# Kernel optimization log

Hardware: AMD Instinct MI355X
Metric: run time of the kernel (lower is better)

## Reference

```python
import jax, jax.numpy as jnp
import numpy as np

N_NODES = 100000
N_EDGES = 1600000
HID = 64
EDGE_DIM = 32
N_LAYERS = 3
BN_EPS = 1e-5


def setup_inputs() -> dict:
    key = jax.random.key(0)
    ks = jax.random.split(key, 8)
    x = jax.random.normal(ks[0], (N_NODES, HID), dtype=jnp.float32)
    edge_index = jax.random.randint(ks[1], (2, N_EDGES), 0, N_NODES, dtype=jnp.int32)
    edge_attr = jax.random.normal(ks[2], (N_EDGES, EDGE_DIM), dtype=jnp.float32)
    s = 0.1  # small init scale for numerical stability
    We = jax.random.normal(ks[3], (N_LAYERS, EDGE_DIM, HID), dtype=jnp.float32) * s
    be = jnp.zeros((N_LAYERS, HID), jnp.float32)
    W1 = jax.random.normal(ks[4], (N_LAYERS, HID, HID), dtype=jnp.float32) * s
    b1 = jnp.zeros((N_LAYERS, HID), jnp.float32)
    W2 = jax.random.normal(ks[5], (N_LAYERS, HID, HID), dtype=jnp.float32) * s
    b2 = jnp.zeros((N_LAYERS, HID), jnp.float32)
    gamma = jnp.ones((N_LAYERS, HID), jnp.float32)
    beta = jnp.zeros((N_LAYERS, HID), jnp.float32)
    Wout = jax.random.normal(ks[6], (HID, HID), dtype=jnp.float32) * s
    bout = jnp.zeros((HID,), jnp.float32)
    return {"x": x, "edge_index": edge_index, "edge_attr": edge_attr,
            "We": We, "be": be, "W1": W1, "b1": b1, "W2": W2, "b2": b2,
            "gamma": gamma, "beta": beta, "Wout": Wout, "bout": bout}


def _forward(x, edge_index, edge_attr, We, be, W1, b1, W2, b2, gamma, beta, Wout, bout):
    src = edge_index[0]  # x_j (source of message)
    dst = edge_index[1]  # aggregation target
    n = x.shape[0]
    for i in range(N_LAYERS):
        # GINEConv: message = relu(x_j + lin_edge(edge_attr)); scatter-add to dst
        e = edge_attr @ We[i] + be[i]                      # [E, H]
        m = jax.nn.relu(x[src] + e)                        # [E, H] (dominant traffic)
        agg = jax.ops.segment_sum(m, dst, num_segments=n)  # [N, H]
        h = x + agg                                        # (1 + eps)*x, eps = 0
        # 2-layer MLP
        h = jax.nn.relu(h @ W1[i] + b1[i]) @ W2[i] + b2[i]
        # BatchNorm1d (training mode: batch statistics, biased variance)
        mean = jnp.mean(h, axis=0)
        var = jnp.var(h, axis=0)
        h = (h - mean) * jax.lax.rsqrt(var + BN_EPS) * gamma[i] + beta[i]
        x = jax.nn.relu(h)
    return x @ Wout + bout


def reference(x, edge_index, edge_attr, We, be, W1, b1, W2, b2, gamma, beta, Wout, bout):
    return _forward(x, edge_index, edge_attr, We, be, W1, b1, W2, b2, gamma, beta, Wout, bout)
```

## Files before the change

kernel.cpp:

```cpp
#include <hip/hip_runtime.h>

#define N_NODES 100000
#define N_EDGES 1600000
#define HID 64
#define EDIM 32
#define BN_EPS 1e-5f

#define SCAN_CHUNK 1024
#define NB_SCAN ((N_NODES + SCAN_CHUNK - 1) / SCAN_CHUNK)

#define G_NODES 16
#define CAP 320

__global__ __launch_bounds__(256) void hist_kernel(
    const int* __restrict__ dst, int* __restrict__ cnt)
{
    int i = (int)(blockIdx.x * blockDim.x + threadIdx.x);
    const int stride = (int)(gridDim.x * blockDim.x);
    for (; i < N_EDGES; i += stride) atomicAdd(&cnt[dst[i]], 1);
}

__global__ __launch_bounds__(256) void scan1_kernel(
    const int* __restrict__ cnt, int* __restrict__ bsum)
{
    __shared__ int s[256];
    const int b = (int)blockIdx.x, t = (int)threadIdx.x;
    const int base = b * SCAN_CHUNK + t * 4;
    int sum = 0;
#pragma unroll
    for (int k = 0; k < 4; ++k) {
        int idx = base + k;
        if (idx < N_NODES) sum += cnt[idx];
    }
    s[t] = sum;
    __syncthreads();
    for (int off = 128; off > 0; off >>= 1) {
        if (t < off) s[t] += s[t + off];
        __syncthreads();
    }
    if (t == 0) bsum[b] = s[0];
}

__global__ __launch_bounds__(128) void scan2_kernel(
    const int* __restrict__ bsum, int* __restrict__ bofs, int* __restrict__ row_ptr)
{
    __shared__ int s[128];
    const int t = (int)threadIdx.x;
    const int v = (t < NB_SCAN) ? bsum[t] : 0;
    s[t] = v;
    __syncthreads();
    for (int off = 1; off < 128; off <<= 1) {
        int add = (t >= off) ? s[t - off] : 0;
        __syncthreads();
        s[t] += add;
        __syncthreads();
    }
    if (t < NB_SCAN) bofs[t] = s[t] - v;
    if (t == NB_SCAN - 1) row_ptr[N_NODES] = s[t];
}

__global__ __launch_bounds__(256) void scan3_kernel(
    const int* __restrict__ cnt, const int* __restrict__ bofs,
    int* __restrict__ row_ptr, int* __restrict__ pos)
{
    __shared__ int s[256];
    const int b = (int)blockIdx.x, t = (int)threadIdx.x;
    const int base = b * SCAN_CHUNK + t * 4;
    int v[4];
    int sum = 0;
#pragma unroll
    for (int k = 0; k < 4; ++k) {
        int idx = base + k;
        v[k] = (idx < N_NODES) ? cnt[idx] : 0;
        sum += v[k];
    }
    s[t] = sum;
    __syncthreads();
    for (int off = 1; off < 256; off <<= 1) {
        int add = (t >= off) ? s[t - off] : 0;
        __syncthreads();
        s[t] += add;
        __syncthreads();
    }
    int run = s[t] - sum + bofs[b];
#pragma unroll
    for (int k = 0; k < 4; ++k) {
        int idx = base + k;
        if (idx < N_NODES) {
            row_ptr[idx] = run;
            pos[idx] = run;
            run += v[k];
        }
    }
}

__global__ __launch_bounds__(256) void scatter_kernel(
    const int* __restrict__ src, const int* __restrict__ dst,
    int* __restrict__ pos, int* __restrict__ perm_e, int* __restrict__ perm_src)
{
    int i = (int)(blockIdx.x * blockDim.x + threadIdx.x);
    const int stride = (int)(gridDim.x * blockDim.x);
    for (; i < N_EDGES; i += stride) {
        const int d = dst[i];
        const int p = atomicAdd(&pos[d], 1);
        perm_e[p] = i;
        perm_src[p] = src[i];
    }
}

__global__ __launch_bounds__(256) void gather_staged_kernel(
    const float* __restrict__ x, const float* __restrict__ eattr,
    const int* __restrict__ row_ptr, const int* __restrict__ perm_e,
    const int* __restrict__ perm_src,
    const float* __restrict__ We, const float* __restrict__ be,
    float* __restrict__ agg)
{
    __shared__ float s_attr[CAP * EDIM];
    __shared__ int   s_src[CAP];

    const int tid  = (int)threadIdx.x;
    const int lane = tid & 63;
    const int w    = tid >> 6;
    const int node_lo = (int)blockIdx.x * G_NODES;

    float wv[EDIM];
#pragma unroll
    for (int k = 0; k < EDIM; ++k) wv[k] = We[k * HID + lane];
    const float bias = be[lane];

    int rp[5];
#pragma unroll
    for (int i = 0; i < 5; ++i) {
        int n = node_lo + 4 * w + i;
        rp[i] = row_ptr[n < N_NODES ? n : N_NODES];
    }
    float acc[4] = {0.0f, 0.0f, 0.0f, 0.0f};

    const int e0 = row_ptr[node_lo < N_NODES ? node_lo : N_NODES];
    const int hi = node_lo + G_NODES;
    const int e1 = row_ptr[hi < N_NODES ? hi : N_NODES];

    for (int c0 = e0; c0 < e1; c0 += CAP) {
        const int cnt = (e1 - c0 < CAP) ? (e1 - c0) : CAP;
        __syncthreads();
        for (int i = tid; i < cnt * 8; i += 256) {
            const int row = i >> 3, part = i & 7;
            const int ep = perm_e[c0 + row];
            ((float4*)s_attr)[i] = ((const float4*)eattr)[(size_t)ep * 8 + part];
        }
        for (int i = tid; i < cnt; i += 256) s_src[i] = perm_src[c0 + i];
        __syncthreads();
        const int c1 = c0 + cnt;

#pragma unroll
        for (int q = 0; q < 4; ++q) {
            const int jb = (rp[q]     > c0) ? rp[q]     : c0;
            const int je = (rp[q + 1] < c1) ? rp[q + 1] : c1;
            float a = acc[q];
            int j = jb;
            if (j < je) {
                int s0 = s_src[j - c0];
                float xv = x[(size_t)s0 * HID + lane];
                while (j < je) {
                    const float4* p = (const float4*)(s_attr + (size_t)(j - c0) * EDIM);
                    const int jn = j + 1;
                    float xn = 0.0f;
                    if (jn < je) {
                        const int sn = s_src[jn - c0];
                        xn = x[(size_t)sn * HID + lane];
                    }
                    float e = bias;
#pragma unroll
                    for (int jj = 0; jj < 8; ++jj) {
                        const float4 qv = p[jj];
                        e = fmaf(qv.x, wv[4 * jj + 0], e);
                        e = fmaf(qv.y, wv[4 * jj + 1], e);
                        e = fmaf(qv.z, wv[4 * jj + 2], e);
                        e = fmaf(qv.w, wv[4 * jj + 3], e);
                    }
                    a += fmaxf(xv + e, 0.0f);
                    xv = xn;
                    j = jn;
                }
            }
            acc[q] = a;
        }
    }

#pragma unroll
    for (int q = 0; q < 4; ++q) {
        const int n = node_lo + 4 * w + q;
        if (n < N_NODES) agg[(size_t)n * HID + lane] = acc[q];
    }
}

__global__ __launch_bounds__(256) void mlp_kernel(
    const float* __restrict__ xin, const float* __restrict__ agg,
    const float* __restrict__ W1, const float* __restrict__ b1,
    const float* __restrict__ W2, const float* __restrict__ b2,
    float* __restrict__ uout)
{
    const int lane = threadIdx.x & 63;
    const int wid  = (int)((blockIdx.x * blockDim.x + threadIdx.x) >> 6);
    const int n    = wid * 64 + lane;
    const bool ok  = (n < N_NODES);
    const size_t base = (size_t)n * HID;

    float h[HID];
    if (ok) {
        const float4* px = (const float4*)(xin + base);
        const float4* pa = (const float4*)(agg + base);
#pragma unroll
        for (int j = 0; j < HID / 4; ++j) {
            float4 xv = px[j];
            float4 av = pa[j];
            h[4 * j + 0] = xv.x + av.x;
            h[4 * j + 1] = xv.y + av.y;
            h[4 * j + 2] = xv.z + av.z;
            h[4 * j + 3] = xv.w + av.w;
        }
    } else {
#pragma unroll
        for (int k = 0; k < HID; ++k) h[k] = 0.0f;
    }

    float u[HID];
#pragma unroll
    for (int f = 0; f < HID; ++f) u[f] = b2[f];

    for (int c = 0; c < 4; ++c) {
        float t[16];
#pragma unroll
        for (int j = 0; j < 16; ++j) t[j] = b1[c * 16 + j];
#pragma unroll
        for (int k = 0; k < HID; ++k) {
            const float hk = h[k];
#pragma unroll
            for (int j = 0; j < 16; ++j)
                t[j] = fmaf(hk, W1[k * HID + c * 16 + j], t[j]);
        }
#pragma unroll
        for (int j = 0; j < 16; ++j) t[j] = fmaxf(t[j], 0.0f);
#pragma unroll
        for (int j = 0; j < 16; ++j) {
            const float tj = t[j];
#pragma unroll
            for (int f = 0; f < HID; ++f)
                u[f] = fmaf(tj, W2[(c * 16 + j) * HID + f], u[f]);
        }
    }

    if (ok) {
        float4* po = (float4*)(uout + base);
#pragma unroll
        for (int j = 0; j < HID / 4; ++j)
            po[j] = make_float4(u[4 * j], u[4 * j + 1], u[4 * j + 2], u[4 * j + 3]);
    }
}

__global__ __launch_bounds__(256) void out_kernel(
    const float* __restrict__ xin, const float* __restrict__ Wo,
    const float* __restrict__ bo, float* __restrict__ out)
{
    const int lane = threadIdx.x & 63;
    const int wid  = (int)((blockIdx.x * blockDim.x + threadIdx.x) >> 6);
    const int n    = wid * 64 + lane;
    const bool ok  = (n < N_NODES);
    const size_t base = (size_t)n * HID;

    float h[HID];
    if (ok) {
        const float4* px = (const float4*)(xin + base);
#pragma unroll
        for (int j = 0; j < HID / 4; ++j) {
            float4 xv = px[j];
            h[4 * j + 0] = xv.x; h[4 * j + 1] = xv.y;
            h[4 * j + 2] = xv.z; h[4 * j + 3] = xv.w;
        }
    } else {
#pragma unroll
        for (int k = 0; k < HID; ++k) h[k] = 0.0f;
    }

    for (int c = 0; c < 4; ++c) {
        float t[16];
#pragma unroll
        for (int j = 0; j < 16; ++j) t[j] = bo[c * 16 + j];
#pragma unroll
        for (int k = 0; k < HID; ++k) {
            const float hk = h[k];
#pragma unroll
            for (int j = 0; j < 16; ++j)
                t[j] = fmaf(hk, Wo[k * HID + c * 16 + j], t[j]);
        }
        if (ok) {
            float4* po = (float4*)(out + base + c * 16);
#pragma unroll
            for (int j = 0; j < 4; ++j)
                po[j] = make_float4(t[4 * j], t[4 * j + 1], t[4 * j + 2], t[4 * j + 3]);
        }
    }
}

__global__ __launch_bounds__(256) void stats_kernel(
    const float* __restrict__ u, float* __restrict__ stats)
{
    __shared__ float ls[256];
    __shared__ float ls2[256];
    const int tid = (int)threadIdx.x;
    const int g   = (int)(blockIdx.x * 256 + tid);
    const int f   = g & 63;
    const int row = g >> 6;
    const int rstride = (int)((gridDim.x * 256) >> 6);

    float s = 0.0f, s2 = 0.0f;
    for (int n = row; n < N_NODES; n += rstride) {
        float v = u[(size_t)n * HID + f];
        s += v;
        s2 = fmaf(v, v, s2);
    }
    ls[tid] = s;
    ls2[tid] = s2;
    __syncthreads();
    if (tid < 64) {
        float a = ls[tid] + ls[tid + 64] + ls[tid + 128] + ls[tid + 192];
        float b = ls2[tid] + ls2[tid + 64] + ls2[tid + 128] + ls2[tid + 192];
        atomicAdd(&stats[tid], a);
        atomicAdd(&stats[64 + tid], b);
    }
}

__global__ __launch_bounds__(256) void bn_relu_kernel(
    const float* __restrict__ u, const float* __restrict__ stats,
    const float* __restrict__ gamma, const float* __restrict__ beta,
    float* __restrict__ xout)
{
    const int total4 = N_NODES * HID / 4;
    int i = (int)(blockIdx.x * blockDim.x + threadIdx.x);
    const int stride = (int)(gridDim.x * blockDim.x);
    const int fb = (i * 4) & 63;

    const float invN = 1.0f / (float)N_NODES;
    float sc[4], sh[4];
#pragma unroll
    for (int j = 0; j < 4; ++j) {
        float mean = stats[fb + j] * invN;
        float var  = stats[64 + fb + j] * invN - mean * mean;
        float s    = gamma[fb + j] * rsqrtf(var + BN_EPS);
        sc[j] = s;
        sh[j] = beta[fb + j] - mean * s;
    }
    for (; i < total4; i += stride) {
        float4 v = ((const float4*)u)[i];
        v.x = fmaxf(fmaf(v.x, sc[0], sh[0]), 0.0f);
        v.y = fmaxf(fmaf(v.y, sc[1], sh[1]), 0.0f);
        v.z = fmaxf(fmaf(v.z, sc[2], sh[2]), 0.0f);
        v.w = fmaxf(fmaf(v.w, sc[3], sh[3]), 0.0f);
        ((float4*)xout)[i] = v;
    }
}

extern "C" void kernel_launch(void* const* d_in, const int* in_sizes, int n_in,
                              void* d_out, int out_size, void* d_ws, size_t ws_size,
                              hipStream_t stream)
{
    const float* x0    = (const float*)d_in[0];
    const int*   eidx  = (const int*)d_in[1];
    const float* eattr = (const float*)d_in[2];
    const float* We    = (const float*)d_in[3];
    const float* be    = (const float*)d_in[4];
    const float* W1    = (const float*)d_in[5];
    const float* b1    = (const float*)d_in[6];
    const float* W2    = (const float*)d_in[7];
    const float* b2    = (const float*)d_in[8];
    const float* gamma = (const float*)d_in[9];
    const float* beta  = (const float*)d_in[10];
    const float* Wout  = (const float*)d_in[11];
    const float* bout  = (const float*)d_in[12];
    float* out = (float*)d_out;

    const int* src = eidx;
    const int* dst = eidx + N_EDGES;

    const size_t NH = (size_t)N_NODES * HID;

    float* A     = (float*)d_ws;
    float* AGG   = A + NH;
    float* stats = AGG + NH;
    int* cnt      = (int*)(stats + 128);
    int* bsum     = cnt + N_NODES;
    int* bofs     = bsum + 128;
    int* row_ptr  = bofs + 128;
    int* pos      = row_ptr + N_NODES + 1;
    int* perm_e   = pos + N_NODES;
    int* perm_src = perm_e + N_EDGES;
    float* B = out;

    hipMemsetAsync(cnt, 0, N_NODES * sizeof(int), stream);
    hist_kernel<<<1024, 256, 0, stream>>>(dst, cnt);
    scan1_kernel<<<NB_SCAN, 256, 0, stream>>>(cnt, bsum);
    scan2_kernel<<<1, 128, 0, stream>>>(bsum, bofs, row_ptr);
    scan3_kernel<<<NB_SCAN, 256, 0, stream>>>(cnt, bofs, row_ptr, pos);
    scatter_kernel<<<1024, 256, 0, stream>>>(src, dst, pos, perm_e, perm_src);

    const int mlp_blocks    = ((N_NODES + 63) / 64 + 3) / 4;
    const int gather_blocks = (N_NODES + G_NODES - 1) / G_NODES;

    const float* xin = x0;
    for (int i = 0; i < 3; ++i) {
        hipMemsetAsync(stats, 0, 128 * sizeof(float), stream);

        gather_staged_kernel<<<gather_blocks, 256, 0, stream>>>(
            xin, eattr, row_ptr, perm_e, perm_src,
            We + (size_t)i * EDIM * HID, be + (size_t)i * HID, AGG);

        mlp_kernel<<<mlp_blocks, 256, 0, stream>>>(
            xin, AGG,
            W1 + (size_t)i * HID * HID, b1 + (size_t)i * HID,
            W2 + (size_t)i * HID * HID, b2 + (size_t)i * HID, B);

        stats_kernel<<<256, 256, 0, stream>>>(B, stats);

        bn_relu_kernel<<<1024, 256, 0, stream>>>(
            B, stats, gamma + (size_t)i * HID, beta + (size_t)i * HID, A);

        xin = A;
    }

    out_kernel<<<mlp_blocks, 256, 0, stream>>>(A, Wout, bout, out);
}
```

Measured before the change: 1.749 ms.

## Stage edge attributes via direct global-to-LDS loads with deeper x prefetch

Edge attributes and source indices are now copied into LDS with global_load_lds, so the data skips registers. The perm_e indices for the next chunk are loaded ahead of time. The chunk size is halved and the kernel gets an occupancy hint of 5 blocks per CU, aiming for more concurrent blocks. x rows are prefetched three edges ahead across the node boundaries inside a chunk, and the 32-term dot product is split into four partial sums to shorten the dependency chain. The trade-offs are more register pressure from the eps array and more chunk iterations with barriers.

```diff
diff --git a/kernel.cpp b/kernel.cpp
--- a/kernel.cpp
+++ b/kernel.cpp
@@ -10,7 +10,10 @@
 #define NB_SCAN ((N_NODES + SCAN_CHUNK - 1) / SCAN_CHUNK)
 
 #define G_NODES 16
-#define CAP 320
+#define CAP 160
+#define S_ATTR_F4 (CAP * 8 + 64)
+#define S_SRC_I   (CAP + 64)
+#define N_EPS ((CAP * 8 + 255) / 256)
 
 __global__ __launch_bounds__(256) void hist_kernel(
     const int* __restrict__ dst, int* __restrict__ cnt)
@@ -108,15 +111,28 @@
     }
 }
 
-__global__ __launch_bounds__(256) void gather_staged_kernel(
+__device__ __forceinline__ void gl_lds16(const float4* g, float4* l)
+{
+    __builtin_amdgcn_global_load_lds(
+        (const __attribute__((address_space(1))) void*)g,
+        (__attribute__((address_space(3))) void*)l, 16, 0, 0);
+}
+__device__ __forceinline__ void gl_lds4(const int* g, int* l)
+{
+    __builtin_amdgcn_global_load_lds(
+        (const __attribute__((address_space(1))) void*)g,
+        (__attribute__((address_space(3))) void*)l, 4, 0, 0);
+}
+
+__global__ __launch_bounds__(256, 5) void gather_staged_kernel(
     const float* __restrict__ x, const float* __restrict__ eattr,
     const int* __restrict__ row_ptr, const int* __restrict__ perm_e,
     const int* __restrict__ perm_src,
     const float* __restrict__ We, const float* __restrict__ be,
     float* __restrict__ agg)
 {
-    __shared__ float s_attr[CAP * EDIM];
-    __shared__ int   s_src[CAP];
+    __shared__ float4 s_attr[S_ATTR_F4];
+    __shared__ int    s_src[S_SRC_I];
 
     const int tid  = (int)threadIdx.x;
     const int lane = tid & 63;
@@ -136,54 +152,93 @@
     }
     float acc[4] = {0.0f, 0.0f, 0.0f, 0.0f};
 
-    const int e0 = row_ptr[node_lo < N_NODES ? node_lo : N_NODES];
+    const int e0 = row_ptr[node_lo];
     const int hi = node_lo + G_NODES;
     const int e1 = row_ptr[hi < N_NODES ? hi : N_NODES];
 
+    const float4* eattr4 = (const float4*)eattr;
+
+    int eps[N_EPS];
+    auto load_eps = [&](int cbase) {
+        const int cc  = (e1 - cbase < CAP) ? (e1 - cbase) : CAP;
+        const int nqq = cc * 8;
+#pragma unroll
+        for (int k = 0; k < N_EPS; ++k) {
+            int i = w * 64 + k * 256 + lane;
+            if (i >= nqq) i = nqq - 1;
+            eps[k] = perm_e[cbase + (i >> 3)];
+        }
+    };
+
+    if (e0 < e1) load_eps(e0);
+
     for (int c0 = e0; c0 < e1; c0 += CAP) {
         const int cnt = (e1 - c0 < CAP) ? (e1 - c0) : CAP;
-        __syncthreads();
-        for (int i = tid; i < cnt * 8; i += 256) {
-            const int row = i >> 3, part = i & 7;
-            const int ep = perm_e[c0 + row];
-            ((float4*)s_attr)[i] = ((const float4*)eattr)[(size_t)ep * 8 + part];
-        }
-        for (int i = tid; i < cnt; i += 256) s_src[i] = perm_src[c0 + i];
-        __syncthreads();
-        const int c1 = c0 + cnt;
-
-#pragma unroll
-        for (int q = 0; q < 4; ++q) {
-            const int jb = (rp[q]     > c0) ? rp[q]     : c0;
-            const int je = (rp[q + 1] < c1) ? rp[q + 1] : c1;
-            float a = acc[q];
-            int j = jb;
-            if (j < je) {
-                int s0 = s_src[j - c0];
-                float xv = x[(size_t)s0 * HID + lane];
-                while (j < je) {
-                    const float4* p = (const float4*)(s_attr + (size_t)(j - c0) * EDIM);
-                    const int jn = j + 1;
-                    float xn = 0.0f;
-                    if (jn < je) {
-                        const int sn = s_src[jn - c0];
-                        xn = x[(size_t)sn * HID + lane];
-                    }
-                    float e = bias;
+        const int nq  = cnt * 8;
+        const int c1  = c0 + cnt;
+
+        __syncthreads();
+
+#pragma unroll
+        for (int k = 0; k < N_EPS; ++k) {
+            const int b = w * 64 + k * 256;
+            if (b < nq) {
+                int i = b + lane;
+                if (i >= nq) i = nq - 1;
+                gl_lds16(eattr4 + (size_t)eps[k] * 8 + (i & 7), s_attr + b);
+            }
+        }
+        {
+            const int b = w * 64;
+            if (b < cnt) {
+                int i = b + lane;
+                if (i >= cnt) i = cnt - 1;
+                gl_lds4(perm_src + c0 + i, s_src + b);
+            }
+        }
+        if (c0 + CAP < e1) load_eps(c0 + CAP);
+
+        __syncthreads();
+
+        int f0 = rp[0] > c0 ? rp[0] : c0;
+        const int F1 = rp[4] < c1 ? rp[4] : c1;
+        if (f0 < F1) {
+            const int FL = F1 - 1;
+            int j1 = (f0 + 1 > FL) ? FL : f0 + 1;
+            int j2 = (f0 + 2 > FL) ? FL : f0 + 2;
+            const int sA = s_src[f0 - c0];
+            const int sB = s_src[j1 - c0];
+            int si = s_src[j2 - c0];
+            float xq0 = x[(size_t)sA * HID + lane];
+            float xq1 = x[(size_t)sB * HID + lane];
+
+#pragma unroll
+            for (int q = 0; q < 4; ++q) {
+                const int jb = (rp[q]     > c0) ? rp[q]     : c0;
+                const int je = (rp[q + 1] < c1) ? rp[q + 1] : c1;
+                float a = acc[q];
+                for (int j = jb; j < je; ++j) {
+                    const float xl = x[(size_t)si * HID + lane];
+                    int j3 = j + 3; if (j3 > FL) j3 = FL;
+                    si = s_src[j3 - c0];
+
+                    const float4* p = s_attr + (size_t)(j - c0) * 8;
+                    float ee[4] = {bias, 0.0f, 0.0f, 0.0f};
 #pragma unroll
                     for (int jj = 0; jj < 8; ++jj) {
                         const float4 qv = p[jj];
-                        e = fmaf(qv.x, wv[4 * jj + 0], e);
-                        e = fmaf(qv.y, wv[4 * jj + 1], e);
-                        e = fmaf(qv.z, wv[4 * jj + 2], e);
-                        e = fmaf(qv.w, wv[4 * jj + 3], e);
+                        float t = ee[jj & 3];
+                        t = fmaf(qv.x, wv[4 * jj + 0], t);
+                        t = fmaf(qv.y, wv[4 * jj + 1], t);
+                        t = fmaf(qv.z, wv[4 * jj + 2], t);
+                        t = fmaf(qv.w, wv[4 * jj + 3], t);
+                        ee[jj & 3] = t;
                     }
-                    a += fmaxf(xv + e, 0.0f);
-                    xv = xn;
-                    j = jn;
+                    a += fmaxf(xq0 + ((ee[0] + ee[1]) + (ee[2] + ee[3])), 0.0f);
+                    xq0 = xq1; xq1 = xl;
                 }
+                acc[q] = a;
             }
-            acc[q] = a;
         }
     }
 
```

After: 1.604 ms. -8.3%, faster.

## Replace LDS-staged edge gather with per-wave scalar-load software pipeline

Applied to the files above, without the earlier changes.

Rewrites the GINE gather kernel. The shared-memory staging of edge attributes and the block-wide barriers are removed. Each wave now walks its four nodes' CSR edge range serially, loading each edge's 32-float attribute row with s_load_dwordx16 into scalar registers. Those loads are double-buffered, and the perm_e, perm_src and x loads run ahead of the current edge. Per-node sums come from differencing one running prefix sum at row boundaries, which avoids per-node loop overhead but can lose some float precision. Scalar-cache throughput and the serial latency chain are the main risks.

```diff
diff --git a/kernel.cpp b/kernel.cpp
--- a/kernel.cpp
+++ b/kernel.cpp
@@ -10,7 +10,8 @@
 #define NB_SCAN ((N_NODES + SCAN_CHUNK - 1) / SCAN_CHUNK)
 
 #define G_NODES 16
-#define CAP 320
+
+typedef __attribute__((ext_vector_type(16))) float f32x16;
 
 __global__ __launch_bounds__(256) void hist_kernel(
     const int* __restrict__ dst, int* __restrict__ cnt)
@@ -108,89 +109,143 @@
     }
 }
 
-__global__ __launch_bounds__(256) void gather_staged_kernel(
+#define SWAIT() do { asm volatile("s_waitcnt lgkmcnt(0)" ::: "memory"); \
+                     __builtin_amdgcn_sched_barrier(0); } while (0)
+
+__device__ __forceinline__ float edge_step(
+    int j, int FL,
+    const float* __restrict__ eattr, const int* __restrict__ perm_e,
+    const int* __restrict__ perm_src, const float* __restrict__ x,
+    int lane, const float* __restrict__ wv, float bias,
+    f32x16& cl, f32x16& ch,
+    f32x16& nl, f32x16& nh,
+    int& eN, int& sN,
+    float& xq0, float& xq1)
+{
+    SWAIT();
+    const float* ap = eattr + (size_t)(unsigned)eN * EDIM;
+    int j2 = j + 2; if (j2 > FL) j2 = FL;
+    int j3 = j + 3; if (j3 > FL) j3 = FL;
+    int e_out, s_out;
+    asm volatile(
+        "s_load_dwordx16 %0, %4, 0x0\n\t"
+        "s_load_dwordx16 %1, %4, 0x40\n\t"
+        "s_load_dword    %2, %5, 0x0\n\t"
+        "s_load_dword    %3, %6, 0x0"
+        : "=&s"(nl), "=&s"(nh), "=&s"(e_out), "=&s"(s_out)
+        : "s"(ap), "s"(perm_e + j2), "s"(perm_src + j3));
+
+    const float xq2 = x[(size_t)(unsigned)sN * HID + lane];
+
+    float ee0 = bias, ee1 = 0.0f, ee2 = 0.0f, ee3 = 0.0f;
+#pragma unroll
+    for (int k = 0; k < 16; k += 4) {
+        ee0 = fmaf(cl[k + 0], wv[k + 0], ee0);
+        ee1 = fmaf(cl[k + 1], wv[k + 1], ee1);
+        ee2 = fmaf(cl[k + 2], wv[k + 2], ee2);
+        ee3 = fmaf(cl[k + 3], wv[k + 3], ee3);
+    }
+#pragma unroll
+    for (int k = 0; k < 16; k += 4) {
+        ee0 = fmaf(ch[k + 0], wv[16 + k + 0], ee0);
+        ee1 = fmaf(ch[k + 1], wv[16 + k + 1], ee1);
+        ee2 = fmaf(ch[k + 2], wv[16 + k + 2], ee2);
+        ee3 = fmaf(ch[k + 3], wv[16 + k + 3], ee3);
+    }
+    const float c = fmaxf(xq0 + ((ee0 + ee1) + (ee2 + ee3)), 0.0f);
+    xq0 = xq1; xq1 = xq2;
+    eN = e_out; sN = s_out;
+    return c;
+}
+
+__global__ __launch_bounds__(256, 6) void gather_csr_kernel(
     const float* __restrict__ x, const float* __restrict__ eattr,
     const int* __restrict__ row_ptr, const int* __restrict__ perm_e,
     const int* __restrict__ perm_src,
     const float* __restrict__ We, const float* __restrict__ be,
     float* __restrict__ agg)
 {
-    __shared__ float s_attr[CAP * EDIM];
-    __shared__ int   s_src[CAP];
-
     const int tid  = (int)threadIdx.x;
     const int lane = tid & 63;
-    const int w    = tid >> 6;
-    const int node_lo = (int)blockIdx.x * G_NODES;
+    const int w    = __builtin_amdgcn_readfirstlane(tid >> 6);
+    const int node_lo = (int)blockIdx.x * G_NODES + 4 * w;
 
     float wv[EDIM];
 #pragma unroll
     for (int k = 0; k < EDIM; ++k) wv[k] = We[k * HID + lane];
     const float bias = be[lane];
 
-    int rp[5];
+    int rpv[5];
 #pragma unroll
     for (int i = 0; i < 5; ++i) {
-        int n = node_lo + 4 * w + i;
-        rp[i] = row_ptr[n < N_NODES ? n : N_NODES];
-    }
-    float acc[4] = {0.0f, 0.0f, 0.0f, 0.0f};
-
-    const int e0 = row_ptr[node_lo < N_NODES ? node_lo : N_NODES];
-    const int hi = node_lo + G_NODES;
-    const int e1 = row_ptr[hi < N_NODES ? hi : N_NODES];
-
-    for (int c0 = e0; c0 < e1; c0 += CAP) {
-        const int cnt = (e1 - c0 < CAP) ? (e1 - c0) : CAP;
-        __syncthreads();
-        for (int i = tid; i < cnt * 8; i += 256) {
-            const int row = i >> 3, part = i & 7;
-            const int ep = perm_e[c0 + row];
-            ((float4*)s_attr)[i] = ((const float4*)eattr)[(size_t)ep * 8 + part];
-        }
-        for (int i = tid; i < cnt; i += 256) s_src[i] = perm_src[c0 + i];
-        __syncthreads();
-        const int c1 = c0 + cnt;
-
-#pragma unroll
-        for (int q = 0; q < 4; ++q) {
-            const int jb = (rp[q]     > c0) ? rp[q]     : c0;
-            const int je = (rp[q + 1] < c1) ? rp[q + 1] : c1;
-            float a = acc[q];
-            int j = jb;
-            if (j < je) {
-                int s0 = s_src[j - c0];
-                float xv = x[(size_t)s0 * HID + lane];
-                while (j < je) {
-                    const float4* p = (const float4*)(s_attr + (size_t)(j - c0) * EDIM);
-                    const int jn = j + 1;
-                    float xn = 0.0f;
-                    if (jn < je) {
-                        const int sn = s_src[jn - c0];
-                        xn = x[(size_t)sn * HID + lane];
-                    }
-                    float e = bias;
-#pragma unroll
-                    for (int jj = 0; jj < 8; ++jj) {
-                        const float4 qv = p[jj];
-                        e = fmaf(qv.x, wv[4 * jj + 0], e);
-                        e = fmaf(qv.y, wv[4 * jj + 1], e);
-                        e = fmaf(qv.z, wv[4 * jj + 2], e);
-                        e = fmaf(qv.w, wv[4 * jj + 3], e);
-                    }
-                    a += fmaxf(xv + e, 0.0f);
-                    xv = xn;
-                    j = jn;
-                }
-            }
-            acc[q] = a;
-        }
-    }
-
+        int n = node_lo + i;
+        n = (n < N_NODES) ? n : N_NODES;
+        rpv[i] = __builtin_amdgcn_readfirstlane(row_ptr[n]);
+    }
+    const int F0 = rpv[0], rp1 = rpv[1], rp2 = rpv[2], rp3 = rpv[3], F1 = rpv[4];
+
+    float a = 0.0f, sn1 = 0.0f, sn2 = 0.0f, sn3 = 0.0f;
+
+    if (F0 < F1) {
+        const int FL = F1 - 1;
+        f32x16 A0, A1, B0, B1;
+        int eN, sN;
+        float xq0, xq1;
+
+        {
+            int jB = F0 + 1; if (jB > FL) jB = FL;
+            int jC = F0 + 2; if (jC > FL) jC = FL;
+            int e0i, eNi, s0i, s1i, sNi;
+            asm volatile(
+                "s_load_dword %0, %5, 0x0\n\t"
+                "s_load_dword %1, %6, 0x0\n\t"
+                "s_load_dword %2, %7, 0x0\n\t"
+                "s_load_dword %3, %8, 0x0\n\t"
+                "s_load_dword %4, %9, 0x0"
+                : "=&s"(e0i), "=&s"(eNi), "=&s"(s0i), "=&s"(s1i), "=&s"(sNi)
+                : "s"(perm_e + F0), "s"(perm_e + jB), "s"(perm_src + F0),
+                  "s"(perm_src + jB), "s"(perm_src + jC));
+            SWAIT();
+            const float* ap0 = eattr + (size_t)(unsigned)e0i * EDIM;
+            asm volatile(
+                "s_load_dwordx16 %0, %2, 0x0\n\t"
+                "s_load_dwordx16 %1, %2, 0x40"
+                : "=&s"(A0), "=&s"(A1) : "s"(ap0));
+            xq0 = x[(size_t)(unsigned)s0i * HID + lane];
+            xq1 = x[(size_t)(unsigned)s1i * HID + lane];
+            eN = eNi; sN = sNi;
+        }
+
+        int j = F0;
+        while (true) {
+            a += edge_step(j, FL, eattr, perm_e, perm_src, x, lane, wv, bias,
+                           A0, A1, B0, B1, eN, sN, xq0, xq1);
+            ++j;
+            if (j == rp1) sn1 = a;
+            if (j == rp2) sn2 = a;
+            if (j == rp3) sn3 = a;
+            if (j >= F1) break;
+
+            a += edge_step(j, FL, eattr, perm_e, perm_src, x, lane, wv, bias,
+                           B0, B1, A0, A1, eN, sN, xq0, xq1);
+            ++j;
+            if (j == rp1) sn1 = a;
+            if (j == rp2) sn2 = a;
+            if (j == rp3) sn3 = a;
+            if (j >= F1) break;
+        }
+        SWAIT();
+    }
+
+    float r[4];
+    r[0] = sn1;
+    r[1] = sn2 - sn1;
+    r[2] = sn3 - sn2;
+    r[3] = a - sn3;
 #pragma unroll
     for (int q = 0; q < 4; ++q) {
-        const int n = node_lo + 4 * w + q;
-        if (n < N_NODES) agg[(size_t)n * HID + lane] = acc[q];
+        const int n = node_lo + q;
+        if (n < N_NODES) agg[(size_t)n * HID + lane] = r[q];
     }
 }
 
@@ -410,7 +465,7 @@
     for (int i = 0; i < 3; ++i) {
         hipMemsetAsync(stats, 0, 128 * sizeof(float), stream);
 
-        gather_staged_kernel<<<gather_blocks, 256, 0, stream>>>(
+        gather_csr_kernel<<<gather_blocks, 256, 0, stream>>>(
             xin, eattr, row_ptr, perm_e, perm_src,
             We + (size_t)i * EDIM * HID, be + (size_t)i * HID, AGG);
 
```

Result: faster. 1.618 ms (-7.5%).

## Pre-permute edge attributes into CSR order and stream gather without LDS staging

Applied to the files above, without the earlier changes.

Adds a one-time kernel that copies edge_attr into dst-sorted order in workspace, so all three layer gathers read attributes linearly instead of through perm_e indirection. The gather kernel drops shared-memory staging and syncthreads. Each wave instead walks its 4 nodes' contiguous edge range with a software-pipelined prefetch of x rows and source indices, and derives per-node sums from running prefix snapshots. It also splits the edge-linear FMA chain into four accumulators and sets a higher occupancy hint. The cost is an extra 200MB permute pass plus workspace use, with a fallback path when the workspace is too small.

```diff
diff --git a/kernel.cpp b/kernel.cpp
--- a/kernel.cpp
+++ b/kernel.cpp
@@ -1,4 +1,5 @@
 #include <hip/hip_runtime.h>
+#include <stdint.h>
 
 #define N_NODES 100000
 #define N_EDGES 1600000
@@ -10,7 +11,6 @@
 #define NB_SCAN ((N_NODES + SCAN_CHUNK - 1) / SCAN_CHUNK)
 
 #define G_NODES 16
-#define CAP 320
 
 __global__ __launch_bounds__(256) void hist_kernel(
     const int* __restrict__ dst, int* __restrict__ cnt)
@@ -108,89 +108,119 @@
     }
 }
 
-__global__ __launch_bounds__(256) void gather_staged_kernel(
-    const float* __restrict__ x, const float* __restrict__ eattr,
+__global__ __launch_bounds__(256) void permute_attr_kernel(
+    const float* __restrict__ eattr, const int* __restrict__ perm_e,
+    float* __restrict__ outp)
+{
+    const int total = N_EDGES * 8;
+    int i = (int)(blockIdx.x * blockDim.x + threadIdx.x);
+    const int stride = (int)(gridDim.x * blockDim.x);
+    for (; i < total; i += stride) {
+        const int row = i >> 3, part = i & 7;
+        ((float4*)outp)[i] =
+            ((const float4*)eattr)[(size_t)(unsigned)perm_e[row] * 8 + part];
+    }
+}
+
+template<bool LINEAR>
+__global__ __launch_bounds__(256, 4) void gather_kernel(
+    const float* __restrict__ x, const float* __restrict__ attr,
     const int* __restrict__ row_ptr, const int* __restrict__ perm_e,
     const int* __restrict__ perm_src,
     const float* __restrict__ We, const float* __restrict__ be,
     float* __restrict__ agg)
 {
-    __shared__ float s_attr[CAP * EDIM];
-    __shared__ int   s_src[CAP];
-
     const int tid  = (int)threadIdx.x;
     const int lane = tid & 63;
-    const int w    = tid >> 6;
-    const int node_lo = (int)blockIdx.x * G_NODES;
-
-    float wv[EDIM];
-#pragma unroll
-    for (int k = 0; k < EDIM; ++k) wv[k] = We[k * HID + lane];
-    const float bias = be[lane];
-
-    int rp[5];
+    const int w    = __builtin_amdgcn_readfirstlane(tid >> 6);
+    const int node_lo = (int)blockIdx.x * G_NODES + 4 * w;
+
+    int rpv[5];
 #pragma unroll
     for (int i = 0; i < 5; ++i) {
-        int n = node_lo + 4 * w + i;
-        rp[i] = row_ptr[n < N_NODES ? n : N_NODES];
-    }
-    float acc[4] = {0.0f, 0.0f, 0.0f, 0.0f};
-
-    const int e0 = row_ptr[node_lo < N_NODES ? node_lo : N_NODES];
-    const int hi = node_lo + G_NODES;
-    const int e1 = row_ptr[hi < N_NODES ? hi : N_NODES];
-
-    for (int c0 = e0; c0 < e1; c0 += CAP) {
-        const int cnt = (e1 - c0 < CAP) ? (e1 - c0) : CAP;
-        __syncthreads();
-        for (int i = tid; i < cnt * 8; i += 256) {
-            const int row = i >> 3, part = i & 7;
-            const int ep = perm_e[c0 + row];
-            ((float4*)s_attr)[i] = ((const float4*)eattr)[(size_t)ep * 8 + part];
-        }
-        for (int i = tid; i < cnt; i += 256) s_src[i] = perm_src[c0 + i];
-        __syncthreads();
-        const int c1 = c0 + cnt;
-
-#pragma unroll
-        for (int q = 0; q < 4; ++q) {
-            const int jb = (rp[q]     > c0) ? rp[q]     : c0;
-            const int je = (rp[q + 1] < c1) ? rp[q + 1] : c1;
-            float a = acc[q];
-            int j = jb;
-            if (j < je) {
-                int s0 = s_src[j - c0];
-                float xv = x[(size_t)s0 * HID + lane];
-                while (j < je) {
-                    const float4* p = (const float4*)(s_attr + (size_t)(j - c0) * EDIM);
-                    const int jn = j + 1;
-                    float xn = 0.0f;
-                    if (jn < je) {
-                        const int sn = s_src[jn - c0];
-                        xn = x[(size_t)sn * HID + lane];
-                    }
-                    float e = bias;
-#pragma unroll
-                    for (int jj = 0; jj < 8; ++jj) {
-                        const float4 qv = p[jj];
-                        e = fmaf(qv.x, wv[4 * jj + 0], e);
-                        e = fmaf(qv.y, wv[4 * jj + 1], e);
-                        e = fmaf(qv.z, wv[4 * jj + 2], e);
-                        e = fmaf(qv.w, wv[4 * jj + 3], e);
-                    }
-                    a += fmaxf(xv + e, 0.0f);
-                    xv = xn;
-                    j = jn;
+        int n = node_lo + i;
+        n = (n < N_NODES) ? n : N_NODES;
+        rpv[i] = __builtin_amdgcn_readfirstlane(row_ptr[n]);
+    }
+    const int F0 = rpv[0], rp1 = rpv[1], rp2 = rpv[2], rp3 = rpv[3], F1 = rpv[4];
+
+    float a = 0.0f, sn1 = 0.0f, sn2 = 0.0f, sn3 = 0.0f;
+
+    if (F0 < F1) {
+        const int FL = F1 - 1;
+
+        float pf_prev;
+        {
+            int gl = F0 + lane; if (gl > FL) gl = FL;
+            size_t row = LINEAR ? (size_t)gl : (size_t)(unsigned)perm_e[gl];
+            pf_prev = attr[row * EDIM];
+        }
+
+        float wv[EDIM];
+#pragma unroll
+        for (int k = 0; k < EDIM; ++k) wv[k] = We[k * HID + lane];
+        const float bias = be[lane];
+
+        int jA = F0;
+        int jB = F0 + 1; if (jB > FL) jB = FL;
+        int jC = F0 + 2; if (jC > FL) jC = FL;
+        const int s0 = perm_src[jA];
+        const int s1 = perm_src[jB];
+        int sN = perm_src[jC];
+        float xq0 = x[(size_t)(unsigned)s0 * HID + lane];
+        float xq1 = x[(size_t)(unsigned)s1 * HID + lane];
+
+        for (int gb = F0; gb < F1; gb += 64) {
+            const int gend = (gb + 64 < F1) ? gb + 64 : F1;
+
+            float pf = 0.0f;
+            if (gb + 64 < F1) {
+                int gl = gb + 64 + lane; if (gl > FL) gl = FL;
+                size_t row = LINEAR ? (size_t)gl : (size_t)(unsigned)perm_e[gl];
+                pf = attr[row * EDIM];
+            }
+
+#pragma unroll 2
+            for (int j = gb; j < gend; ++j) {
+                const float xq2 = x[(size_t)(unsigned)sN * HID + lane];
+                int j3 = j + 3; if (j3 > FL) j3 = FL;
+                sN = perm_src[j3];
+
+                size_t row = LINEAR ? (size_t)j : (size_t)(unsigned)perm_e[j];
+                const float4* ap = (const float4*)(attr + row * EDIM);
+
+                float e0 = bias, e1 = 0.0f, e2 = 0.0f, e3 = 0.0f;
+#pragma unroll
+                for (int k = 0; k < 8; ++k) {
+                    const float4 q = ap[k];
+                    e0 = fmaf(q.x, wv[4 * k + 0], e0);
+                    e1 = fmaf(q.y, wv[4 * k + 1], e1);
+                    e2 = fmaf(q.z, wv[4 * k + 2], e2);
+                    e3 = fmaf(q.w, wv[4 * k + 3], e3);
                 }
+                a += fmaxf(xq0 + ((e0 + e1) + (e2 + e3)), 0.0f);
+                xq0 = xq1; xq1 = xq2;
+
+                if (j + 1 == rp1) sn1 = a;
+                if (j + 1 == rp2) sn2 = a;
+                if (j + 1 == rp3) sn3 = a;
             }
-            acc[q] = a;
-        }
-    }
-
+
+            asm volatile("" :: "v"(pf_prev));
+            pf_prev = pf;
+        }
+        asm volatile("" :: "v"(pf_prev));
+    }
+
+    float r[4];
+    r[0] = sn1;
+    r[1] = sn2 - sn1;
+    r[2] = sn3 - sn2;
+    r[3] = a - sn3;
 #pragma unroll
     for (int q = 0; q < 4; ++q) {
-        const int n = node_lo + 4 * w + q;
-        if (n < N_NODES) agg[(size_t)n * HID + lane] = acc[q];
+        const int n = node_lo + q;
+        if (n < N_NODES) agg[(size_t)n * HID + lane] = r[q];
     }
 }
 
@@ -396,12 +426,20 @@
     int* perm_src = perm_e + N_EDGES;
     float* B = out;
 
+    uintptr_t eap_off = (((uintptr_t)(perm_src + N_EDGES) - (uintptr_t)d_ws)
+                         + 255) & ~(uintptr_t)255;
+    const size_t need = (size_t)eap_off + (size_t)N_EDGES * EDIM * sizeof(float);
+    const bool lin = (ws_size >= need);
+    float* EAP = (float*)((char*)d_ws + eap_off);
+
     hipMemsetAsync(cnt, 0, N_NODES * sizeof(int), stream);
     hist_kernel<<<1024, 256, 0, stream>>>(dst, cnt);
     scan1_kernel<<<NB_SCAN, 256, 0, stream>>>(cnt, bsum);
     scan2_kernel<<<1, 128, 0, stream>>>(bsum, bofs, row_ptr);
     scan3_kernel<<<NB_SCAN, 256, 0, stream>>>(cnt, bofs, row_ptr, pos);
     scatter_kernel<<<1024, 256, 0, stream>>>(src, dst, pos, perm_e, perm_src);
+    if (lin)
+        permute_attr_kernel<<<2048, 256, 0, stream>>>(eattr, perm_e, EAP);
 
     const int mlp_blocks    = ((N_NODES + 63) / 64 + 3) / 4;
     const int gather_blocks = (N_NODES + G_NODES - 1) / G_NODES;
@@ -410,9 +448,14 @@
     for (int i = 0; i < 3; ++i) {
         hipMemsetAsync(stats, 0, 128 * sizeof(float), stream);
 
-        gather_staged_kernel<<<gather_blocks, 256, 0, stream>>>(
-            xin, eattr, row_ptr, perm_e, perm_src,
-            We + (size_t)i * EDIM * HID, be + (size_t)i * HID, AGG);
+        if (lin)
+            gather_kernel<true><<<gather_blocks, 256, 0, stream>>>(
+                xin, EAP, row_ptr, perm_e, perm_src,
+                We + (size_t)i * EDIM * HID, be + (size_t)i * HID, AGG);
+        else
+            gather_kernel<false><<<gather_blocks, 256, 0, stream>>>(
+                xin, eattr, row_ptr, perm_e, perm_src,
+                We + (size_t)i * EDIM * HID, be + (size_t)i * HID, AGG);
 
         mlp_kernel<<<mlp_blocks, 256, 0, stream>>>(
             xin, AGG,
```

New measurement: 1.477 ms. 15.6% less time.
